# Performance work log

Hardware: AMD Instinct MI355X
Metric: run time of the kernel (lower is better)

Reference implementation:

```python
import jax, jax.numpy as jnp
import numpy as np

B, L, C, H = 2, 2048, 2048, 16
COND = 2048
HID = 4 * C
LN_EPS = 1e-6


def _ln(x):
    m = jnp.mean(x, axis=-1, keepdims=True)
    v = jnp.mean((x - m) ** 2, axis=-1, keepdims=True)
    return (x - m) / jnp.sqrt(v + LN_EPS)


def _gelu_tanh(u):
    c = np.sqrt(2.0 / np.pi).astype(np.float32)
    return 0.5 * u * (1.0 + jnp.tanh(c * (u + 0.044715 * u ** 3)))


def setup_inputs() -> dict:
    key = jax.random.key(0)
    ks = jax.random.split(key, 8)
    s = 0.02
    return {
        "x": jax.random.normal(ks[0], (B, L, C), jnp.float32),
        "cond_BD": jax.random.normal(ks[1], (B, COND), jnp.float32),
        "attn_bias": jnp.zeros((1, 1, L, L), jnp.float32),
        "Wqkv": (jax.random.normal(ks[2], (3 * C, C), jnp.float32) * s),
        "q_bias": jnp.zeros((C,), jnp.float32),
        "v_bias": jnp.zeros((C,), jnp.float32),
        "scale_mul_log": jnp.full((1, H, 1, 1), np.log(4.0), jnp.float32),
        "Wproj": (jax.random.normal(ks[3], (C, C), jnp.float32) * s),
        "bproj": jnp.zeros((C,), jnp.float32),
        "Wada": (jax.random.normal(ks[4], (6 * C, COND), jnp.float32) * s),
        "bada": jnp.zeros((6 * C,), jnp.float32),
        "Wfc1": (jax.random.normal(ks[5], (HID, C), jnp.float32) * s),
        "bfc1": jnp.zeros((HID,), jnp.float32),
        "Wfc2": (jax.random.normal(ks[6], (C, HID), jnp.float32) * s),
        "bfc2": jnp.zeros((C,), jnp.float32),
    }


def reference(x, cond_BD, attn_bias, Wqkv, q_bias, v_bias, scale_mul_log,
              Wproj, bproj, Wada, bada, Wfc1, bfc1, Wfc2, bfc2):
    Bs, Lx, Cx = x.shape
    D = Cx // H
    # AdaLN modulation: SiLU -> Linear(cond_dim, 6C) -> view(B,1,6,C).unbind(2)
    ada = (jax.nn.silu(cond_BD) @ Wada.T + bada).reshape(Bs, 1, 6, Cx)
    gamma1, gamma2, scale1, scale2, shift1, shift2 = [ada[:, :, i, :] for i in range(6)]

    def attn(xin):
        qkv_bias = jnp.concatenate([q_bias, jnp.zeros_like(q_bias), v_bias])
        qkv = (xin @ Wqkv.T + qkv_bias).reshape(Bs, Lx, 3, H, D)
        qkv = jnp.transpose(qkv, (2, 0, 3, 1, 4))  # [3, B, H, L, D]
        q, k, v = qkv[0], qkv[1], qkv[2]
        # cos-attn: L2-normalize q,k; q scaled by exp(clamped log-scale); softmax scale = 1
        sm = jnp.exp(jnp.minimum(scale_mul_log, jnp.log(jnp.float32(100.0))))
        qn = q / jnp.maximum(jnp.linalg.norm(q, axis=-1, keepdims=True), 1e-12) * sm
        kn = k / jnp.maximum(jnp.linalg.norm(k, axis=-1, keepdims=True), 1e-12)
        scores = jnp.einsum('bhqd,bhkd->bhqk', qn, kn) + attn_bias
        p = jax.nn.softmax(scores, axis=-1)
        o = jnp.einsum('bhqk,bhkd->bhqd', p, v)
        o = jnp.transpose(o, (0, 2, 1, 3)).reshape(Bs, Lx, Cx)
        return o @ Wproj.T + bproj

    x = x + attn(_ln(x) * (scale1 + 1.0) + shift1) * gamma1
    h = _gelu_tanh((_ln(x) * (scale2 + 1.0) + shift2) @ Wfc1.T + bfc1)
    x = x + (h @ Wfc2.T + bfc2) * gamma2
    return x
```

## Files before the change

kernel.cpp:

```cpp
#include <hip/hip_runtime.h>

typedef unsigned short u16;
typedef float f32x4 __attribute__((ext_vector_type(4)));
typedef short short8 __attribute__((ext_vector_type(8)));

#define C_ 2048
#define L_ 2048
#define H_ 16
#define D_ 128
#define SIXC 12288

__device__ __forceinline__ u16 f2bf(float f) {
  union { float f; unsigned u; } v; v.f = f;
  unsigned r = v.u + 0x7FFFu + ((v.u >> 16) & 1u);
  return (u16)(r >> 16);
}
__device__ __forceinline__ float bf2f(u16 b) {
  union { unsigned u; float f; } v; v.u = ((unsigned)b) << 16; return v.f;
}

#define GLOAD_LDS16(g, l)                                            \
  __builtin_amdgcn_global_load_lds(                                  \
      (__attribute__((address_space(1))) void*)(g),                  \
      (__attribute__((address_space(3))) void*)(l), 16, 0, 0)

template <int N> __device__ __forceinline__ void wait_vmcnt() {
  if constexpr (N == 8)      asm volatile("s_waitcnt vmcnt(8)" ::: "memory");
  else if constexpr (N == 6) asm volatile("s_waitcnt vmcnt(6)" ::: "memory");
  else                       asm volatile("s_waitcnt vmcnt(0)" ::: "memory");
}

__global__ __launch_bounds__(256) void conv_bf16(
    const float* __restrict__ src, u16* __restrict__ dst, int n) {
  int i = (blockIdx.x * 256 + threadIdx.x) * 4;
  if (i >= n) return;
  float4 v = *(const float4*)&src[i];
  ushort4 o;
  o.x = f2bf(v.x); o.y = f2bf(v.y); o.z = f2bf(v.z); o.w = f2bf(v.w);
  *(ushort4*)&dst[i] = o;
}

__global__ __launch_bounds__(256) void prep_kernel(
    const float* __restrict__ cond, const float* __restrict__ qb,
    const float* __restrict__ vb, const float* __restrict__ sml,
    float* __restrict__ silu_cond, float* __restrict__ qkvbias,
    float* __restrict__ sm) {
  int i = blockIdx.x * 256 + threadIdx.x;
  if (i < 4096) { float c = cond[i]; silu_cond[i] = c / (1.f + __expf(-c)); }
  if (i < 6144) {
    float bv = (i < 2048) ? qb[i] : ((i < 4096) ? 0.f : vb[i - 4096]);
    qkvbias[i] = bv;
  }
  if (i < 16) sm[i] = __expf(fminf(sml[i], 4.6051701859880914f));
}

__global__ __launch_bounds__(256) void ada_gemm(
    const float* __restrict__ sc, const float* __restrict__ Wada,
    const float* __restrict__ bada, float* __restrict__ ada) {
  int gw = (blockIdx.x * 256 + threadIdx.x) >> 6;
  int lane = threadIdx.x & 63;
  int b = gw / SIXC, row = gw % SIXC;
  const float* s0 = sc + b * 2048;
  const float* w0 = Wada + (size_t)row * 2048;
  float s = 0.f;
  for (int k = lane * 4; k < 2048; k += 256) {
    float4 a = *(const float4*)&s0[k];
    float4 w = *(const float4*)&w0[k];
    s = fmaf(a.x, w.x, s); s = fmaf(a.y, w.y, s);
    s = fmaf(a.z, w.z, s); s = fmaf(a.w, w.w, s);
  }
  #pragma unroll
  for (int off = 32; off; off >>= 1) s += __shfl_xor(s, off);
  if (lane == 0) ada[(size_t)b * SIXC + row] = s + bada[row];
}

__global__ __launch_bounds__(256) void ln_mod(
    const float* __restrict__ x, const float* __restrict__ ada,
    u16* __restrict__ out, int soff, int shoff) {
  int r = blockIdx.x;
  int b = r >> 11;
  int tid = threadIdx.x;
  const float* xr = x + (size_t)r * 2048;
  int c0 = tid * 8;
  float4 u0 = *(const float4*)&xr[c0];
  float4 u1 = *(const float4*)&xr[c0 + 4];
  float v[8] = {u0.x,u0.y,u0.z,u0.w,u1.x,u1.y,u1.z,u1.w};
  float s = 0.f, s2 = 0.f;
  #pragma unroll
  for (int j = 0; j < 8; ++j) { s += v[j]; s2 = fmaf(v[j], v[j], s2); }
  int wv = tid >> 6, lane = tid & 63;
  #pragma unroll
  for (int off = 32; off; off >>= 1) { s += __shfl_xor(s, off); s2 += __shfl_xor(s2, off); }
  __shared__ float red[8];
  if (!lane) { red[wv] = s; red[4 + wv] = s2; }
  __syncthreads();
  s = red[0] + red[1] + red[2] + red[3];
  s2 = red[4] + red[5] + red[6] + red[7];
  float mean = s * (1.f / 2048.f);
  float var = s2 * (1.f / 2048.f) - mean * mean;
  float rstd = rsqrtf(var + 1e-6f);
  const float* sc = ada + (size_t)b * SIXC + soff;
  const float* sh = ada + (size_t)b * SIXC + shoff;
  u16* orow = out + (size_t)r * 2048;
  #pragma unroll
  for (int j = 0; j < 8; ++j) {
    int c = c0 + j;
    float y = (v[j] - mean) * rstd * (1.f + sc[c]) + sh[c];
    orow[c] = f2bf(y);
  }
}

__global__ __launch_bounds__(256) void qk_norm_bf(
    u16* __restrict__ qb, u16* __restrict__ kb, const float* __restrict__ sm) {
  int gw = (blockIdx.x * 256 + threadIdx.x) >> 6;
  int lane = threadIdx.x & 63;
  int which = gw >> 16;
  int rid = gw & 0xFFFF;
  int h = (rid >> 11) & 15;
  u16* base = (which ? kb : qb) + (size_t)rid * 128 + lane * 2;
  unsigned uu = *(const unsigned*)base;
  float v0 = bf2f((u16)(uu & 0xFFFFu));
  float v1 = bf2f((u16)(uu >> 16));
  float ss = v0 * v0 + v1 * v1;
  #pragma unroll
  for (int off = 32; off; off >>= 1) ss += __shfl_xor(ss, off);
  float rn = 1.f / fmaxf(sqrtf(ss), 1e-12f);
  if (which == 0) rn *= sm[h];
  unsigned o = (unsigned)f2bf(v0 * rn) | ((unsigned)f2bf(v1 * rn) << 16);
  *(unsigned*)base = o;
}

#define PSP 68
__global__ __launch_bounds__(256) void attn_mfma(
    const u16* __restrict__ qb, const u16* __restrict__ kb,
    const u16* __restrict__ vbt, const float* __restrict__ bias,
    u16* __restrict__ o) {
  __shared__ u16 Ks[2][64 * 128];
  __shared__ u16 Vt[2][128 * 64];
  __shared__ u16 Ps[4][16 * PSP];
  int tid = threadIdx.x;
  int w = tid >> 6, lane = tid & 63;
  int flat = blockIdx.y * gridDim.x + blockIdx.x;
  int rl = (flat & 7) * 128 + (flat >> 3);
  int bh = rl >> 5, b = bh >> 4, h = bh & 15;
  int q0 = (rl & 31) * 64;
  int lr = lane & 15, lg = lane >> 4;
  short8 aq[4];
  {
    const u16* qrow = qb + ((size_t)bh * L_ + q0 + w * 16 + lr) * 128 + lg * 8;
    #pragma unroll
    for (int ks = 0; ks < 4; ++ks) aq[ks] = *(const short8*)(qrow + ks * 32);
  }
  f32x4 oacc[8] = {};
  float m = -1e30f, l = 0.f;
  const float* brow = bias + (size_t)(q0 + w * 16 + lr) * L_;
  const u16* kbase = kb + (size_t)bh * L_ * 128;
  const u16* vbase = vbt + (size_t)bh * 128 * L_;
  const int kq0 = tid;
  const int vq0 = tid;

  float4 brg[4], bnr[4];
  #pragma unroll
  for (int i = 0; i < 4; ++i) {
    int q = i * 256 + kq0;
    int r = q >> 4, c = q & 15;
    GLOAD_LDS16(kbase + (size_t)r * 128 + ((c ^ (r & 7)) * 8), &Ks[0][q * 8]);
  }
  #pragma unroll
  for (int i = 0; i < 4; ++i) {
    int q = i * 256 + vq0;
    int r = q >> 3, c = q & 7;
    GLOAD_LDS16(vbase + (size_t)r * L_ + ((c ^ (r & 7)) * 8), &Vt[0][q * 8]);
  }
  #pragma unroll
  for (int kg = 0; kg < 4; ++kg)
    brg[kg] = *(const float4*)&brow[kg * 16 + lg * 4];
  __syncthreads();

  for (int kt = 0; kt < 32; ++kt) {
    const int cur = kt & 1;
    if (kt < 31) {
      const int nxt = cur ^ 1;
      const u16* kb2 = kbase + (size_t)(kt + 1) * 64 * 128;
      #pragma unroll
      for (int i = 0; i < 4; ++i) {
        int q = i * 256 + kq0;
        int r = q >> 4, c = q & 15;
        GLOAD_LDS16(kb2 + (size_t)r * 128 + ((c ^ (r & 7)) * 8), &Ks[nxt][q * 8]);
      }
      #pragma unroll
      for (int i = 0; i < 4; ++i) {
        int q = i * 256 + vq0;
        int r = q >> 3, c = q & 7;
        GLOAD_LDS16(vbase + (size_t)r * L_ + (kt + 1) * 64 + ((c ^ (r & 7)) * 8),
                    &Vt[nxt][q * 8]);
      }
      #pragma unroll
      for (int kg = 0; kg < 4; ++kg)
        bnr[kg] = *(const float4*)&brow[(kt + 1) * 64 + kg * 16 + lg * 4];
    }
    f32x4 s[4] = {};
    __builtin_amdgcn_s_setprio(1);
    #pragma unroll
    for (int ks = 0; ks < 4; ++ks) {
      #pragma unroll
      for (int kg = 0; kg < 4; ++kg) {
        int row = kg * 16 + lr;
        short8 bk = *(const short8*)&Ks[cur][row * 128 + (((ks * 4 + lg) ^ (lr & 7)) * 8)];
        s[kg] = __builtin_amdgcn_mfma_f32_16x16x32_bf16(bk, aq[ks], s[kg], 0, 0, 0);
      }
    }
    __builtin_amdgcn_s_setprio(0);
    float p[4][4];
    #pragma unroll
    for (int kg = 0; kg < 4; ++kg) {
      p[kg][0] = s[kg][0] + brg[kg].x;
      p[kg][1] = s[kg][1] + brg[kg].y;
      p[kg][2] = s[kg][2] + brg[kg].z;
      p[kg][3] = s[kg][3] + brg[kg].w;
    }
    float tm = fmaxf(
        fmaxf(fmaxf(fmaxf(p[0][0], p[0][1]), fmaxf(p[0][2], p[0][3])),
              fmaxf(fmaxf(p[1][0], p[1][1]), fmaxf(p[1][2], p[1][3]))),
        fmaxf(fmaxf(fmaxf(p[2][0], p[2][1]), fmaxf(p[2][2], p[2][3])),
              fmaxf(fmaxf(p[3][0], p[3][1]), fmaxf(p[3][2], p[3][3]))));
    tm = fmaxf(tm, __shfl_xor(tm, 16));
    tm = fmaxf(tm, __shfl_xor(tm, 32));
    if (__any(tm > m + 8.f)) {
      float nm = fmaxf(m, tm);
      float a = __expf(m - nm);
      m = nm;
      l *= a;
      float al[4];
      #pragma unroll
      for (int j = 0; j < 4; ++j) al[j] = __shfl(a, lg * 4 + j);
      #pragma unroll
      for (int dg = 0; dg < 8; ++dg) {
        f32x4 t = oacc[dg];
        t[0] *= al[0]; t[1] *= al[1]; t[2] *= al[2]; t[3] *= al[3];
        oacc[dg] = t;
      }
    }
    float ps = 0.f;
    #pragma unroll
    for (int kg = 0; kg < 4; ++kg) {
      #pragma unroll
      for (int j = 0; j < 4; ++j) { p[kg][j] = __expf(p[kg][j] - m); ps += p[kg][j]; }
    }
    ps += __shfl_xor(ps, 16);
    ps += __shfl_xor(ps, 32);
    l += ps;
    #pragma unroll
    for (int kg = 0; kg < 4; ++kg) {
      unsigned lo = (unsigned)f2bf(p[kg][0]) | ((unsigned)f2bf(p[kg][1]) << 16);
      unsigned hi = (unsigned)f2bf(p[kg][2]) | ((unsigned)f2bf(p[kg][3]) << 16);
      uint2 w2; w2.x = lo; w2.y = hi;
      *(uint2*)&Ps[w][lr * PSP + kg * 16 + lg * 4] = w2;
    }
    __threadfence_block();
    short8 pa0 = *(const short8*)&Ps[w][lr * PSP + lg * 8];
    short8 pa1 = *(const short8*)&Ps[w][lr * PSP + 32 + lg * 8];
    __builtin_amdgcn_s_setprio(1);
    #pragma unroll
    for (int dg = 0; dg < 8; ++dg) {
      int row = dg * 16 + lr;
      short8 bv0 = *(const short8*)&Vt[cur][row * 64 + ((lg ^ (lr & 7)) * 8)];
      oacc[dg] = __builtin_amdgcn_mfma_f32_16x16x32_bf16(pa0, bv0, oacc[dg], 0, 0, 0);
      short8 bv1 = *(const short8*)&Vt[cur][row * 64 + (((4 + lg) ^ (lr & 7)) * 8)];
      oacc[dg] = __builtin_amdgcn_mfma_f32_16x16x32_bf16(pa1, bv1, oacc[dg], 0, 0, 0);
    }
    __builtin_amdgcn_s_setprio(0);
    __syncthreads();
    #pragma unroll
    for (int i = 0; i < 4; ++i) brg[i] = bnr[i];
  }
  float inv[4];
  #pragma unroll
  for (int j = 0; j < 4; ++j) inv[j] = 1.f / __shfl(l, lg * 4 + j);
  #pragma unroll
  for (int j = 0; j < 4; ++j) {
    u16* dst = &o[((size_t)(b * L_) + q0 + w * 16 + lg * 4 + j) * 2048 + h * 128 + lr];
    #pragma unroll
    for (int dg = 0; dg < 8; ++dg) dst[dg * 16] = f2bf(oacc[dg][j] * inv[j]);
  }
}

template <int BM, int EPI>
__global__ __launch_bounds__(512, 2) void gemm8p(
    const u16* __restrict__ A, const u16* __restrict__ W,
    const float* __restrict__ bias, const float* __restrict__ res,
    const float* __restrict__ ada, int goff,
    float* __restrict__ outf, u16* __restrict__ outb,
    u16* __restrict__ p0, u16* __restrict__ p1, u16* __restrict__ p2,
    int M, int N, int K) {
  constexpr int MI  = BM / 32;
  constexpr int MIH = MI / 2;
  constexpr int LA  = BM / 64;
  constexpr int VMW = LA + 4;
  __shared__ __attribute__((aligned(16))) u16 As[2][BM * 64];
  __shared__ __attribute__((aligned(16))) u16 Bs[2][256 * 64];
  const int tid = threadIdx.x;
  const int m0 = blockIdx.y * BM, n0 = blockIdx.x * 256;
  const int wv = tid >> 6, lane = tid & 63;
  const int wr = wv >> 2, wc = wv & 3;
  const int lr = lane & 15, lg = lane >> 4;
  const int sr = lane >> 3;
  const int scol = ((lane & 7) ^ sr) * 8;
  const int cswz = (lr & 7) * 8;
  f32x4 acc[MI][4] = {};
  const u16* Ab = A + (size_t)m0 * K;
  const u16* Bb = W + (size_t)n0 * K;
  const int nt = K >> 6;

  auto stage = [&](int bi, int k0) {
    #pragma unroll
    for (int p = 0; p < LA; ++p) {
      int chunk = wv * LA + p;
      int row = chunk * 8 + sr;
      GLOAD_LDS16(Ab + (size_t)row * K + k0 + scol, &As[bi][chunk * 512]);
    }
    #pragma unroll
    for (int p = 0; p < 4; ++p) {
      int chunk = wv * 4 + p;
      int row = chunk * 8 + sr;
      GLOAD_LDS16(Bb + (size_t)row * K + k0 + scol, &Bs[bi][chunk * 512]);
    }
  };

  stage(0, 0);
  for (int t = 0; t < nt; ++t) {
    const int cur = t & 1;
    if (t + 1 < nt) {
      stage(cur ^ 1, (t + 1) << 6);
      wait_vmcnt<VMW>();
    } else {
      wait_vmcnt<0>();
    }
    __builtin_amdgcn_s_barrier();
    __builtin_amdgcn_sched_barrier(0);
    short8 bf[4][2];
    #pragma unroll
    for (int mh = 0; mh < 2; ++mh) {
      short8 af[MIH][2];
      #pragma unroll
      for (int kk = 0; kk < 2; ++kk) {
        const int col = (kk * 32 + lg * 8) ^ cswz;
        #pragma unroll
        for (int i = 0; i < MIH; ++i)
          af[i][kk] = *(const short8*)
              &As[cur][(wr * (BM / 2) + (mh * MIH + i) * 16 + lr) * 64 + col];
        if (mh == 0) {
          #pragma unroll
          for (int i = 0; i < 4; ++i)
            bf[i][kk] = *(const short8*)
                &Bs[cur][(wc * 64 + i * 16 + lr) * 64 + col];
        }
      }
      asm volatile("s_waitcnt lgkmcnt(0)" ::: "memory");
      __builtin_amdgcn_sched_barrier(0);
      if constexpr (BM == 256) {
        #pragma unroll
        for (int nh = 0; nh < 2; ++nh) {
          __builtin_amdgcn_s_setprio(1);
          #pragma unroll
          for (int kk = 0; kk < 2; ++kk)
            #pragma unroll
            for (int i = 0; i < MIH; ++i)
              #pragma unroll
              for (int jn = 0; jn < 2; ++jn)
                acc[mh * MIH + i][nh * 2 + jn] =
                    __builtin_amdgcn_mfma_f32_16x16x32_bf16(
                        af[i][kk], bf[nh * 2 + jn][kk],
                        acc[mh * MIH + i][nh * 2 + jn], 0, 0, 0);
          __builtin_amdgcn_s_setprio(0);
          __builtin_amdgcn_s_barrier();
        }
      } else {
        __builtin_amdgcn_s_setprio(1);
        #pragma unroll
        for (int kk = 0; kk < 2; ++kk)
          #pragma unroll
          for (int i = 0; i < MIH; ++i)
            #pragma unroll
            for (int jn = 0; jn < 4; ++jn)
              acc[mh * MIH + i][jn] = __builtin_amdgcn_mfma_f32_16x16x32_bf16(
                  af[i][kk], bf[jn][kk], acc[mh * MIH + i][jn], 0, 0, 0);
        __builtin_amdgcn_s_setprio(0);
        __builtin_amdgcn_s_barrier();
      }
    }
    __builtin_amdgcn_sched_barrier(0);
  }
  #pragma unroll
  for (int mi = 0; mi < MI; ++mi) {
    #pragma unroll
    for (int ni = 0; ni < 4; ++ni) {
      int gcol = n0 + wc * 64 + ni * 16 + lr;
      float bv = bias[gcol];
      #pragma unroll
      for (int j = 0; j < 4; ++j) {
        int grow = m0 + wr * (BM / 2) + mi * 16 + lg * 4 + j;
        float v = acc[mi][ni][j] + bv;
        if constexpr (EPI == 0) {
          int which = gcol >> 11;
          int h = (gcol >> 7) & 15;
          int d = gcol & 127;
          int b = grow >> 11, ll = grow & 2047;
          int bh = b * 16 + h;
          if (which == 0)      p0[((size_t)bh * L_ + ll) * 128 + d] = f2bf(v);
          else if (which == 1) p1[((size_t)bh * L_ + ll) * 128 + d] = f2bf(v);
          else                 p2[((size_t)bh * 128 + d) * L_ + ll] = f2bf(v);
        } else if constexpr (EPI == 1) {
          float u = 0.7978845608028654f * (v + 0.044715f * v * v * v);
          float e = __expf(2.f * u);
          float th = 1.f - 2.f / (e + 1.f);
          outb[(size_t)grow * N + gcol] = f2bf(0.5f * v * (1.f + th));
        } else {
          int b = grow >> 11;
          float g = ada[(size_t)b * SIXC + goff + gcol];
          size_t oi = (size_t)grow * N + gcol;
          outf[oi] = res[oi] + v * g;
        }
      }
    }
  }
}

extern "C" void kernel_launch(void* const* d_in, const int* in_sizes, int n_in,
                              void* d_out, int out_size, void* d_ws, size_t ws_size,
                              hipStream_t stream) {
  const float* x        = (const float*)d_in[0];
  const float* cond     = (const float*)d_in[1];
  const float* attnbias = (const float*)d_in[2];
  const float* Wqkv     = (const float*)d_in[3];
  const float* q_bias   = (const float*)d_in[4];
  const float* v_bias   = (const float*)d_in[5];
  const float* sml      = (const float*)d_in[6];
  const float* Wproj    = (const float*)d_in[7];
  const float* bproj    = (const float*)d_in[8];
  const float* Wada     = (const float*)d_in[9];
  const float* bada     = (const float*)d_in[10];
  const float* Wfc1     = (const float*)d_in[11];
  const float* bfc1     = (const float*)d_in[12];
  const float* Wfc2     = (const float*)d_in[13];
  const float* bfc2     = (const float*)d_in[14];
  float* out = (float*)d_out;
  char* ws = (char*)d_ws;
  const size_t MB = 1ull << 20;

  float* silu_cond = (float*)(ws + 0);
  float* qkvbias   = (float*)(ws + (16 << 10));
  float* smbuf     = (float*)(ws + (40 << 10));
  float* adab      = (float*)(ws + (48 << 10));
  u16*   xob       = (u16*)(ws + 1 * MB);
  u16*   qbb       = (u16*)(ws + 17 * MB);
  u16*   kbb       = (u16*)(ws + 33 * MB);
  float* x1        = (float*)(ws + 17 * MB);
  u16*   vbt       = (u16*)(ws + 49 * MB);
  u16*   hbuf      = (u16*)(ws + 49 * MB);
  u16*   wqkv_bf   = (u16*)(ws + 65 * MB);
  u16*   wproj_bf  = (u16*)(ws + 89 * MB);
  u16*   wfc1_bf   = (u16*)(ws + 113 * MB);
  u16*   wfc2_bf   = (u16*)(ws + 145 * MB);

  conv_bf16<<<12288, 256, 0, stream>>>(Wqkv, wqkv_bf, 6144 * 2048);
  conv_bf16<<<4096, 256, 0, stream>>>(Wproj, wproj_bf, 2048 * 2048);
  conv_bf16<<<16384, 256, 0, stream>>>(Wfc1, wfc1_bf, 8192 * 2048);
  conv_bf16<<<16384, 256, 0, stream>>>(Wfc2, wfc2_bf, 2048 * 8192);
  prep_kernel<<<24, 256, 0, stream>>>(cond, q_bias, v_bias, sml, silu_cond, qkvbias, smbuf);
  ada_gemm<<<6144, 256, 0, stream>>>(silu_cond, Wada, bada, adab);
  ln_mod<<<4096, 256, 0, stream>>>(x, adab, xob, 2 * C_, 4 * C_);
  gemm8p<256, 0><<<dim3(24, 16), 512, 0, stream>>>(xob, wqkv_bf, qkvbias, nullptr, nullptr, 0,
      nullptr, nullptr, qbb, kbb, vbt, 4096, 6144, 2048);
  qk_norm_bf<<<32768, 256, 0, stream>>>(qbb, kbb, smbuf);
  attn_mfma<<<dim3(32, 32), 256, 0, stream>>>(qbb, kbb, vbt, attnbias, xob);
  gemm8p<128, 2><<<dim3(8, 32), 512, 0, stream>>>(xob, wproj_bf, bproj, x, adab, 0,
      x1, nullptr, nullptr, nullptr, nullptr, 4096, 2048, 2048);
  ln_mod<<<4096, 256, 0, stream>>>(x1, adab, xob, 3 * C_, 5 * C_);
  gemm8p<256, 1><<<dim3(32, 16), 512, 0, stream>>>(xob, wfc1_bf, bfc1, nullptr, nullptr, 0,
      nullptr, hbuf, nullptr, nullptr, nullptr, 4096, 8192, 2048);
  gemm8p<128, 2><<<dim3(8, 32), 512, 0, stream>>>(hbuf, wfc2_bf, bfc2, x1, adab, C_,
      out, nullptr, nullptr, nullptr, nullptr, 4096, 2048, 8192);
}
```

Before: 908.2 us.

## Restructure GEMM main loop into phased ping-pong schedule with XCD-aware block swizzle

Rewrites the bf16 GEMM main loop so that two tiles are prefetched up front and the next global-to-LDS stage is issued mid-iteration, after the buffer's earlier MFMA phases and before its final one. LDS fragment reads are split per quadrant and interleaved with barrier-fenced MFMA phases. Separately, workgroup IDs are remapped so consecutive tiles land on the same XCD for better L2 reuse. This aims to overlap global loads with compute and cut L2 misses. In exchange it adds more barriers and a tighter dependence on the vmcnt counts being correct.

```diff
diff --git a/kernel.cpp b/kernel.cpp
--- a/kernel.cpp
+++ b/kernel.cpp
@@ -285,22 +285,68 @@
   }
 }
 
+#define PH_PRE                                                \
+  __builtin_amdgcn_sched_barrier(0);                          \
+  __builtin_amdgcn_s_barrier();                               \
+  asm volatile("s_waitcnt lgkmcnt(0)" ::: "memory");          \
+  __builtin_amdgcn_sched_barrier(0);                          \
+  __builtin_amdgcn_s_setprio(1)
+#define PH_POST                                               \
+  __builtin_amdgcn_s_setprio(0);                              \
+  __builtin_amdgcn_sched_barrier(0);                          \
+  __builtin_amdgcn_s_barrier()
+
+#define COLK(kk) (((kk) * 32 + lg * 8) ^ cswz)
+
+#define RD_A256(mh)                                                          \
+  _Pragma("unroll") for (int kk = 0; kk < 2; ++kk)                           \
+  _Pragma("unroll") for (int i = 0; i < 4; ++i)                              \
+    af[i][kk] = *(const short8*)                                             \
+        &As[cur][(wr * 128 + (mh) * 64 + i * 16 + lr) * 64 + COLK(kk)];
+
+#define RD_A128()                                                            \
+  _Pragma("unroll") for (int kk = 0; kk < 2; ++kk)                           \
+  _Pragma("unroll") for (int i = 0; i < 4; ++i)                              \
+    af[i][kk] = *(const short8*)                                             \
+        &As[cur][(wr * 64 + i * 16 + lr) * 64 + COLK(kk)];
+
+#define RD_B(nh, BB)                                                         \
+  _Pragma("unroll") for (int kk = 0; kk < 2; ++kk)                           \
+  _Pragma("unroll") for (int j = 0; j < 2; ++j)                              \
+    BB[j][kk] = *(const short8*)                                             \
+        &Bs[cur][(wc * 64 + ((nh) * 2 + j) * 16 + lr) * 64 + COLK(kk)];
+
+#define MFMA_Q256(mh, nh, BB)                                                \
+  _Pragma("unroll") for (int kk = 0; kk < 2; ++kk)                           \
+  _Pragma("unroll") for (int i = 0; i < 4; ++i)                              \
+  _Pragma("unroll") for (int j = 0; j < 2; ++j)                              \
+    acc[(mh) * 4 + i][(nh) * 2 + j] = __builtin_amdgcn_mfma_f32_16x16x32_bf16(\
+        af[i][kk], BB[j][kk], acc[(mh) * 4 + i][(nh) * 2 + j], 0, 0, 0);
+
+#define MFMA_H128(nh, BB)                                                    \
+  _Pragma("unroll") for (int kk = 0; kk < 2; ++kk)                           \
+  _Pragma("unroll") for (int i = 0; i < 4; ++i)                              \
+  _Pragma("unroll") for (int j = 0; j < 2; ++j)                              \
+    acc[i][(nh) * 2 + j] = __builtin_amdgcn_mfma_f32_16x16x32_bf16(          \
+        af[i][kk], BB[j][kk], acc[i][(nh) * 2 + j], 0, 0, 0);
+
 template <int BM, int EPI>
-__global__ __launch_bounds__(512, 2) void gemm8p(
+__global__ __launch_bounds__(512, 2) void gemm4p(
     const u16* __restrict__ A, const u16* __restrict__ W,
     const float* __restrict__ bias, const float* __restrict__ res,
     const float* __restrict__ ada, int goff,
     float* __restrict__ outf, u16* __restrict__ outb,
     u16* __restrict__ p0, u16* __restrict__ p1, u16* __restrict__ p2,
     int M, int N, int K) {
-  constexpr int MI  = BM / 32;
-  constexpr int MIH = MI / 2;
-  constexpr int LA  = BM / 64;
-  constexpr int VMW = LA + 4;
+  constexpr int MI = BM / 32;
+  constexpr int LA = BM / 64;
   __shared__ __attribute__((aligned(16))) u16 As[2][BM * 64];
   __shared__ __attribute__((aligned(16))) u16 Bs[2][256 * 64];
   const int tid = threadIdx.x;
-  const int m0 = blockIdx.y * BM, n0 = blockIdx.x * 256;
+  const int nwg = gridDim.x * gridDim.y;
+  const int flat = blockIdx.y * gridDim.x + blockIdx.x;
+  const int swz = (flat & 7) * (nwg >> 3) + (flat >> 3);
+  const int m0 = (swz / gridDim.x) * BM, n0 = (swz % gridDim.x) * 256;
   const int wv = tid >> 6, lane = tid & 63;
   const int wr = wv >> 2, wc = wv & 3;
   const int lr = lane & 15, lg = lane >> 4;
@@ -327,70 +373,42 @@
     }
   };
 
+  short8 af[4][2], bf0[2][2], bf1[2][2];
   stage(0, 0);
-  for (int t = 0; t < nt; ++t) {
-    const int cur = t & 1;
-    if (t + 1 < nt) {
-      stage(cur ^ 1, (t + 1) << 6);
-      wait_vmcnt<VMW>();
-    } else {
-      wait_vmcnt<0>();
-    }
-    __builtin_amdgcn_s_barrier();
-    __builtin_amdgcn_sched_barrier(0);
-    short8 bf[4][2];
-    #pragma unroll
-    for (int mh = 0; mh < 2; ++mh) {
-      short8 af[MIH][2];
-      #pragma unroll
-      for (int kk = 0; kk < 2; ++kk) {
-        const int col = (kk * 32 + lg * 8) ^ cswz;
-        #pragma unroll
-        for (int i = 0; i < MIH; ++i)
-          af[i][kk] = *(const short8*)
-              &As[cur][(wr * (BM / 2) + (mh * MIH + i) * 16 + lr) * 64 + col];
-        if (mh == 0) {
-          #pragma unroll
-          for (int i = 0; i < 4; ++i)
-            bf[i][kk] = *(const short8*)
-                &Bs[cur][(wc * 64 + i * 16 + lr) * 64 + col];
-        }
-      }
-      asm volatile("s_waitcnt lgkmcnt(0)" ::: "memory");
+  stage(1, 64);
+  wait_vmcnt<LA + 4>();
+  __builtin_amdgcn_s_barrier();
+
+  if constexpr (BM == 256) {
+    for (int t = 0; t < nt; ++t) {
+      const int cur = t & 1;
+      RD_A256(0); RD_B(0, bf0);
+      PH_PRE; MFMA_Q256(0, 0, bf0); PH_POST;
+      RD_B(1, bf1);
+      PH_PRE; MFMA_Q256(0, 1, bf1); PH_POST;
+      RD_A256(1);
+      PH_PRE; MFMA_Q256(1, 0, bf0); PH_POST;
+      if (t + 2 < nt) stage(cur, (t + 2) << 6);
+      if (t + 1 < nt) { if (t + 2 < nt) wait_vmcnt<8>(); else wait_vmcnt<0>(); }
       __builtin_amdgcn_sched_barrier(0);
-      if constexpr (BM == 256) {
-        #pragma unroll
-        for (int nh = 0; nh < 2; ++nh) {
-          __builtin_amdgcn_s_setprio(1);
-          #pragma unroll
-          for (int kk = 0; kk < 2; ++kk)
-            #pragma unroll
-            for (int i = 0; i < MIH; ++i)
-              #pragma unroll
-              for (int jn = 0; jn < 2; ++jn)
-                acc[mh * MIH + i][nh * 2 + jn] =
-                    __builtin_amdgcn_mfma_f32_16x16x32_bf16(
-                        af[i][kk], bf[nh * 2 + jn][kk],
-                        acc[mh * MIH + i][nh * 2 + jn], 0, 0, 0);
-          __builtin_amdgcn_s_setprio(0);
-          __builtin_amdgcn_s_barrier();
-        }
-      } else {
-        __builtin_amdgcn_s_setprio(1);
-        #pragma unroll
-        for (int kk = 0; kk < 2; ++kk)
-          #pragma unroll
-          for (int i = 0; i < MIH; ++i)
-            #pragma unroll
-            for (int jn = 0; jn < 4; ++jn)
-              acc[mh * MIH + i][jn] = __builtin_amdgcn_mfma_f32_16x16x32_bf16(
-                  af[i][kk], bf[jn][kk], acc[mh * MIH + i][jn], 0, 0, 0);
-        __builtin_amdgcn_s_setprio(0);
-        __builtin_amdgcn_s_barrier();
-      }
-    }
-    __builtin_amdgcn_sched_barrier(0);
-  }
+      __builtin_amdgcn_s_setprio(1);
+      MFMA_Q256(1, 1, bf1);
+      PH_POST;
+    }
+  } else {
+    for (int t = 0; t < nt; ++t) {
+      const int cur = t & 1;
+      RD_A128(); RD_B(0, bf0); RD_B(1, bf1);
+      PH_PRE; MFMA_H128(0, bf0); PH_POST;
+      if (t + 2 < nt) stage(cur, (t + 2) << 6);
+      if (t + 1 < nt) { if (t + 2 < nt) wait_vmcnt<6>(); else wait_vmcnt<0>(); }
+      __builtin_amdgcn_sched_barrier(0);
+      __builtin_amdgcn_s_setprio(1);
+      MFMA_H128(1, bf1);
+      PH_POST;
+    }
+  }
+
   #pragma unroll
   for (int mi = 0; mi < MI; ++mi) {
     #pragma unroll
@@ -470,15 +488,15 @@
   prep_kernel<<<24, 256, 0, stream>>>(cond, q_bias, v_bias, sml, silu_cond, qkvbias, smbuf);
   ada_gemm<<<6144, 256, 0, stream>>>(silu_cond, Wada, bada, adab);
   ln_mod<<<4096, 256, 0, stream>>>(x, adab, xob, 2 * C_, 4 * C_);
-  gemm8p<256, 0><<<dim3(24, 16), 512, 0, stream>>>(xob, wqkv_bf, qkvbias, nullptr, nullptr, 0,
+  gemm4p<256, 0><<<dim3(24, 16), 512, 0, stream>>>(xob, wqkv_bf, qkvbias, nullptr, nullptr, 0,
       nullptr, nullptr, qbb, kbb, vbt, 4096, 6144, 2048);
   qk_norm_bf<<<32768, 256, 0, stream>>>(qbb, kbb, smbuf);
   attn_mfma<<<dim3(32, 32), 256, 0, stream>>>(qbb, kbb, vbt, attnbias, xob);
-  gemm8p<128, 2><<<dim3(8, 32), 512, 0, stream>>>(xob, wproj_bf, bproj, x, adab, 0,
+  gemm4p<128, 2><<<dim3(8, 32), 512, 0, stream>>>(xob, wproj_bf, bproj, x, adab, 0,
       x1, nullptr, nullptr, nullptr, nullptr, 4096, 2048, 2048);
   ln_mod<<<4096, 256, 0, stream>>>(x1, adab, xob, 3 * C_, 5 * C_);
-  gemm8p<256, 1><<<dim3(32, 16), 512, 0, stream>>>(xob, wfc1_bf, bfc1, nullptr, nullptr, 0,
+  gemm4p<256, 1><<<dim3(32, 16), 512, 0, stream>>>(xob, wfc1_bf, bfc1, nullptr, nullptr, 0,
       nullptr, hbuf, nullptr, nullptr, nullptr, 4096, 8192, 2048);
-  gemm8p<128, 2><<<dim3(8, 32), 512, 0, stream>>>(hbuf, wfc2_bf, bfc2, x1, adab, C_,
+  gemm4p<128, 2><<<dim3(8, 32), 512, 0, stream>>>(hbuf, wfc2_bf, bfc2, x1, adab, C_,
       out, nullptr, nullptr, nullptr, nullptr, 4096, 2048, 8192);
 }
```

Result: faster. 839.5 us (-7.6%).
